# Kernel optimization log

Hardware: AMD Instinct MI355X
Metric: run time of the kernel (lower is better)

The kernel has to match this reference:

```python
import jax, jax.numpy as jnp
import numpy as np

T, H, I, E, TOPK = 4096, 2880, 2880, 16, 4
EPS = 1e-5
ALPHA = 1.702


def setup_inputs() -> dict:
    key = jax.random.key(0)
    ks = jax.random.split(key, 8)
    s = 0.02
    return {
        "x": jax.random.normal(ks[0], (T, H), dtype=jnp.float32),
        "norm_w": jnp.ones((H,), dtype=jnp.float32),
        "gate_w": jax.random.normal(ks[1], (E, H), dtype=jnp.float32) * s,
        "gate_b": jax.random.normal(ks[2], (E,), dtype=jnp.float32) * s,
        "w1": jax.random.normal(ks[3], (E, 2 * I, H), dtype=jnp.float32) * s,  # fused gate_up
        "b1": jax.random.normal(ks[4], (E, 2 * I), dtype=jnp.float32) * s,
        "w2": jax.random.normal(ks[5], (E, H, I), dtype=jnp.float32) * s,      # down proj
        "b2": jax.random.normal(ks[6], (E, H), dtype=jnp.float32) * s,
    }


def _rmsnorm(x, w, eps=EPS):
    var = jnp.mean(x * x, axis=-1, keepdims=True)
    return x * jax.lax.rsqrt(var + eps) * w


def _swiglu(gu):
    glu, lin = jnp.split(gu, 2, axis=-1)
    return glu * jax.nn.sigmoid(ALPHA * glu) * (lin + 1.0)


def reference(x, norm_w, gate_w, gate_b, w1, b1, w2, b2):
    t = _rmsnorm(x, norm_w)                       # [T, H]
    logits = t @ gate_w.T + gate_b                # [T, E]
    # Renormalize routing: top-k of logits, softmax over the k selected logits
    vals, idx = jax.lax.top_k(logits, TOPK)       # [T, k]
    wts = jax.nn.softmax(vals, axis=-1)           # [T, k]
    combine = jnp.zeros((t.shape[0], E), dtype=t.dtype)
    combine = combine.at[jnp.arange(t.shape[0])[:, None], idx].set(wts)  # [T, E]
    out = jnp.zeros_like(x)
    for e in range(E):                            # small fixed expert loop
        gu = t @ w1[e].T + b1[e]                  # [T, 2I]
        y = _swiglu(gu) @ w2[e].T + b2[e]         # [T, H]
        out = out + combine[:, e:e + 1] * y
    return x + out
```

## Files before the change

kernel.cpp:

```cpp
#include <hip/hip_runtime.h>
#include <hip/hip_bf16.h>
#include <math.h>
#include <stdint.h>

#define T_TOK 4096
#define H_DIM 2880
#define E_NUM 16
#define ALPHA 1.702f
#define EPS_RMS 1e-5f

#define PADM 192
#define BK 32
#define NK (H_DIM / BK)
#define MAX_RT 104
#define MAX_ROWS (MAX_RT * PADM)
#define NCT1 30
#define NCT2 15
#define G1 (MAX_RT * NCT1)
#define G2 (MAX_RT * NCT2)

typedef __attribute__((ext_vector_type(8))) short short8;
typedef __attribute__((ext_vector_type(4))) float f32x4;

__device__ __forceinline__ unsigned short f2bf(float f) {
  unsigned u = __float_as_uint(f);
  return (unsigned short)((u + 0x7fffu + ((u >> 16) & 1u)) >> 16);
}
__device__ __forceinline__ unsigned pk2(float a, float b) {
  return (unsigned)f2bf(a) | ((unsigned)f2bf(b) << 16);
}
__device__ __forceinline__ void gl_lds16(const void* g, unsigned char* lds_dst) {
  __builtin_amdgcn_global_load_lds(
      (const __attribute__((address_space(1))) void*)g,
      (__attribute__((address_space(3))) void*)lds_dst, 16, 0, 0);
}

__global__ __launch_bounds__(256) void k_norm_gate(
    const float* __restrict__ x, const float* __restrict__ norm_w,
    const float* __restrict__ gate_w, const float* __restrict__ gate_b,
    float* __restrict__ out, unsigned short* __restrict__ t_out,
    int* __restrict__ topk_id, float* __restrict__ topk_w,
    int* __restrict__ counts)
{
  int t = blockIdx.x, tid = threadIdx.x;
  const float4* xr = (const float4*)(x + (size_t)t * H_DIM);
  float4* outr = (float4*)(out + (size_t)t * H_DIM);
  float4 xa[3];
  float ss = 0.f;
  int j = 0;
  for (int i = tid; i < 720; i += 256, j++) {
    float4 v = xr[i]; xa[j] = v; outr[i] = v;
    ss += v.x * v.x + v.y * v.y + v.z * v.z + v.w * v.w;
  }
#pragma unroll
  for (int o = 1; o < 64; o <<= 1) ss += __shfl_xor(ss, o, 64);
  __shared__ float red[4];
  if ((tid & 63) == 0) red[tid >> 6] = ss;
  __syncthreads();
  float rs = rsqrtf((red[0] + red[1] + red[2] + red[3]) * (1.f / H_DIM) + EPS_RMS);

  float part[16];
#pragma unroll
  for (int q = 0; q < 16; q++) part[q] = 0.f;
  j = 0;
  for (int i = tid; i < 720; i += 256, j++) {
    float4 v = xa[j];
    float4 w = ((const float4*)norm_w)[i];
    float t0 = v.x * rs * w.x, t1 = v.y * rs * w.y;
    float t2 = v.z * rs * w.z, t3 = v.w * rs * w.w;
    ushort4 b; b.x = f2bf(t0); b.y = f2bf(t1); b.z = f2bf(t2); b.w = f2bf(t3);
    ((ushort4*)(t_out + (size_t)t * H_DIM))[i] = b;
#pragma unroll
    for (int q = 0; q < 16; q++) {
      float4 g = ((const float4*)(gate_w + (size_t)q * H_DIM))[i];
      part[q] += t0 * g.x + t1 * g.y + t2 * g.z + t3 * g.w;
    }
  }
  __shared__ float lg[4][16];
#pragma unroll
  for (int q = 0; q < 16; q++) {
    float p = part[q];
#pragma unroll
    for (int o = 1; o < 64; o <<= 1) p += __shfl_xor(p, o, 64);
    if ((tid & 63) == 0) lg[tid >> 6][q] = p;
  }
  __syncthreads();
  if (tid == 0) {
    float logit[16];
    for (int q = 0; q < 16; q++)
      logit[q] = lg[0][q] + lg[1][q] + lg[2][q] + lg[3][q] + gate_b[q];
    unsigned used = 0; int idx[4]; float val[4];
    for (int k = 0; k < 4; k++) {
      float best = -3.4e38f; int bi = 0;
      for (int q = 0; q < 16; q++)
        if (!((used >> q) & 1u) && logit[q] > best) { best = logit[q]; bi = q; }
      used |= 1u << bi; idx[k] = bi; val[k] = best;
    }
    float s0 = 0.f, w4[4];
    for (int k = 0; k < 4; k++) { w4[k] = expf(val[k] - val[0]); s0 += w4[k]; }
    for (int k = 0; k < 4; k++) {
      topk_id[t * 4 + k] = idx[k];
      topk_w[t * 4 + k] = w4[k] / s0;
      atomicAdd(&counts[idx[k]], 1);
    }
  }
}

__global__ void k_offsets(const int* __restrict__ counts, int* __restrict__ d_off) {
  if (threadIdx.x == 0) {
    int acc = 0;
    for (int q = 0; q < 16; q++) {
      d_off[q] = acc;
      acc += ((counts[q] + PADM - 1) / PADM) * PADM;
    }
    d_off[16] = acc;
  }
}

__global__ __launch_bounds__(256) void k_fill(
    const int* __restrict__ topk_id, const float* __restrict__ topk_w,
    const int* __restrict__ counts, const int* __restrict__ d_off,
    int* __restrict__ perm_tok, float* __restrict__ perm_w)
{
  int e = blockIdx.x;
  int base = d_off[e], pe = d_off[e + 1] - base, cnt = counts[e];
  int tid = threadIdx.x, lane = tid & 63, wv = tid >> 6;
  __shared__ int wsum[4];
  int pos = 0;
  for (int c0 = 0; c0 < T_TOK; c0 += 256) {
    int tok = c0 + tid;
    int4 ids = ((const int4*)topk_id)[tok];
    int flag = 0, slot = 0;
    if (ids.x == e) { flag = 1; slot = 0; }
    else if (ids.y == e) { flag = 1; slot = 1; }
    else if (ids.z == e) { flag = 1; slot = 2; }
    else if (ids.w == e) { flag = 1; slot = 3; }
    unsigned long long b = __ballot(flag);
    int wprefix = __popcll(b & ((1ULL << lane) - 1ULL));
    if (lane == 0) wsum[wv] = __popcll(b);
    __syncthreads();
    int woff = 0;
    for (int i = 0; i < wv; i++) woff += wsum[i];
    int tot = wsum[0] + wsum[1] + wsum[2] + wsum[3];
    if (flag) {
      int p = base + pos + woff + wprefix;
      perm_tok[p] = tok;
      perm_w[p] = topk_w[tok * 4 + slot];
    }
    pos += tot;
    __syncthreads();
  }
  for (int i = cnt + tid; i < pe; i += 256) {
    perm_tok[base + i] = 0;
    perm_w[base + i] = 0.f;
  }
}

__global__ __launch_bounds__(256, 2) void k_gemm1(
    const unsigned short* __restrict__ t_bf16,
    const float* __restrict__ w1, const float* __restrict__ b1,
    const int* __restrict__ perm_tok, const int* __restrict__ d_off,
    unsigned short* __restrict__ act)
{
  __shared__ __align__(16) unsigned char lds[49152];
  const int total = d_off[16];
  int bid = blockIdx.x;
  int wg = (bid & 7) * (G1 / 8) + (bid >> 3);
  int ct = wg / MAX_RT, rt = wg % MAX_RT;
  int rowbase = rt * PADM;
  if (rowbase >= total) return;
  int e = 0;
#pragma unroll
  for (int q = 0; q < E_NUM; q++) if (d_off[q + 1] <= rowbase) e = q + 1;

  int tid = threadIdx.x, lane = tid & 63, wv = tid >> 6;

  const unsigned short* asrc[3]; unsigned adst[3];
#pragma unroll
  for (int i = 0; i < 3; i++) {
    int cl = tid + 256 * i;
    int r = cl >> 2, c = cl & 3;
    int cs = c ^ ((r >> 1) & 3);
    int tok = perm_tok[rowbase + r];
    asrc[i] = t_bf16 + (size_t)tok * H_DIM + cs * 8;
    adst[i] = (unsigned)cl * 16;
  }
  const float4* bsrc[3]; unsigned bdst[3];
#pragma unroll
  for (int j = 0; j < 3; j++) {
    int idx = tid + 256 * j;
    int r = idx >> 2, c = idx & 3;
    size_t grow = (size_t)e * (2 * H_DIM) +
                  (r < 96 ? (size_t)(ct * 96 + r) : (size_t)(H_DIM + ct * 96 + (r - 96)));
    bsrc[j] = (const float4*)(w1 + grow * H_DIM) + c * 2;
    bdst[j] = (unsigned)(24576 + r * 64 + ((c ^ ((r >> 1) & 3)) << 4));
  }

  int ch = lane >> 4;
  unsigned aoff[3], boff[12];
#pragma unroll
  for (int m = 0; m < 3; m++) {
    int r = wv * 48 + m * 16 + (lane & 15);
    aoff[m] = (unsigned)(r * 64 + ((ch ^ ((r >> 1) & 3)) << 4));
  }
#pragma unroll
  for (int n = 0; n < 12; n++) {
    int r = n * 16 + (lane & 15);
    boff[n] = (unsigned)(24576 + r * 64 + ((ch ^ ((r >> 1) & 3)) << 4));
  }

  f32x4 zero = {0.f, 0.f, 0.f, 0.f};
  f32x4 acc[3][12];
#pragma unroll
  for (int m = 0; m < 3; m++)
#pragma unroll
    for (int n = 0; n < 12; n++) acc[m][n] = zero;

  float4 bv[3][2];
#pragma unroll
  for (int i = 0; i < 3; i++) gl_lds16(asrc[i], lds + adst[i]);
#pragma unroll
  for (int j = 0; j < 3; j++) { bv[j][0] = bsrc[j][0]; bv[j][1] = bsrc[j][1]; }
#pragma unroll
  for (int j = 0; j < 3; j++) {
    uint4 p;
    p.x = pk2(bv[j][0].x, bv[j][0].y); p.y = pk2(bv[j][0].z, bv[j][0].w);
    p.z = pk2(bv[j][1].x, bv[j][1].y); p.w = pk2(bv[j][1].z, bv[j][1].w);
    *(uint4*)(lds + bdst[j]) = p;
  }
  __syncthreads();

  int cur = 0;
  for (int kk = 0; kk < NK; kk++) {
    int nxt = cur ^ 1;
    if (kk + 1 < NK) {
#pragma unroll
      for (int i = 0; i < 3; i++)
        gl_lds16(asrc[i] + (size_t)(kk + 1) * BK, lds + nxt * 12288 + adst[i]);
#pragma unroll
      for (int j = 0; j < 3; j++) {
        bv[j][0] = bsrc[j][(kk + 1) * 8];
        bv[j][1] = bsrc[j][(kk + 1) * 8 + 1];
      }
    }
    const unsigned char* Ab = lds + cur * 12288;
    short8 a[3];
#pragma unroll
    for (int m = 0; m < 3; m++) a[m] = *(const short8*)(Ab + aoff[m]);
    __builtin_amdgcn_s_setprio(1);
#pragma unroll
    for (int n = 0; n < 12; n++) {
      short8 b = *(const short8*)(lds + cur * 12288 + boff[n]);
#pragma unroll
      for (int m = 0; m < 3; m++)
        acc[m][n] = __builtin_amdgcn_mfma_f32_16x16x32_bf16(a[m], b, acc[m][n], 0, 0, 0);
    }
    __builtin_amdgcn_s_setprio(0);
    if (kk + 1 < NK) {
#pragma unroll
      for (int j = 0; j < 3; j++) {
        uint4 p;
        p.x = pk2(bv[j][0].x, bv[j][0].y); p.y = pk2(bv[j][0].z, bv[j][0].w);
        p.z = pk2(bv[j][1].x, bv[j][1].y); p.w = pk2(bv[j][1].z, bv[j][1].w);
        *(uint4*)(lds + nxt * 12288 + bdst[j]) = p;
      }
    }
    __syncthreads();
    cur = nxt;
  }

  int colL = lane & 15, rq = lane >> 4;
#pragma unroll
  for (int m = 0; m < 3; m++) {
    int row0 = rowbase + wv * 48 + m * 16 + rq * 4;
#pragma unroll
    for (int n = 0; n < 6; n++) {
      int col = ct * 96 + n * 16 + colL;
      float bg = b1[(size_t)e * (2 * H_DIM) + col];
      float bl = b1[(size_t)e * (2 * H_DIM) + H_DIM + col];
#pragma unroll
      for (int j = 0; j < 4; j++) {
        float g = acc[m][n][j] + bg;
        float l = acc[m][n + 6][j] + bl;
        float s = 1.f / (1.f + __expf(-ALPHA * g));
        act[(size_t)(row0 + j) * H_DIM + col] = f2bf(g * s * (l + 1.f));
      }
    }
  }
}

__global__ __launch_bounds__(256, 2) void k_gemm2(
    const unsigned short* __restrict__ act,
    const float* __restrict__ w2, const float* __restrict__ b2,
    const int* __restrict__ perm_tok, const float* __restrict__ perm_w,
    const int* __restrict__ d_off,
    float* __restrict__ out)
{
  __shared__ __align__(16) unsigned char lds[49152];
  __shared__ int stok[PADM]; __shared__ float swt[PADM];
  const int total = d_off[16];
  int bid = blockIdx.x;
  int wg = (bid & 7) * (G2 / 8) + (bid >> 3);
  int ct = wg / MAX_RT, rt = wg % MAX_RT;
  int rowbase = rt * PADM;
  if (rowbase >= total) return;
  int e = 0;
#pragma unroll
  for (int q = 0; q < E_NUM; q++) if (d_off[q + 1] <= rowbase) e = q + 1;

  int tid = threadIdx.x, lane = tid & 63, wv = tid >> 6;
  if (tid < PADM) { stok[tid] = perm_tok[rowbase + tid]; swt[tid] = perm_w[rowbase + tid]; }

  const unsigned short* asrc[3]; unsigned adst[3];
#pragma unroll
  for (int i = 0; i < 3; i++) {
    int cl = tid + 256 * i;
    int r = cl >> 2, c = cl & 3;
    int cs = c ^ ((r >> 1) & 3);
    asrc[i] = act + (size_t)(rowbase + r) * H_DIM + cs * 8;
    adst[i] = (unsigned)cl * 16;
  }
  const float4* bsrc[3]; unsigned bdst[3];
#pragma unroll
  for (int j = 0; j < 3; j++) {
    int idx = tid + 256 * j;
    int r = idx >> 2, c = idx & 3;
    size_t grow = (size_t)e * H_DIM + (size_t)(ct * PADM + r);
    bsrc[j] = (const float4*)(w2 + grow * H_DIM) + c * 2;
    bdst[j] = (unsigned)(24576 + r * 64 + ((c ^ ((r >> 1) & 3)) << 4));
  }

  int ch = lane >> 4;
  unsigned aoff[3], boff[12];
#pragma unroll
  for (int m = 0; m < 3; m++) {
    int r = wv * 48 + m * 16 + (lane & 15);
    aoff[m] = (unsigned)(r * 64 + ((ch ^ ((r >> 1) & 3)) << 4));
  }
#pragma unroll
  for (int n = 0; n < 12; n++) {
    int r = n * 16 + (lane & 15);
    boff[n] = (unsigned)(24576 + r * 64 + ((ch ^ ((r >> 1) & 3)) << 4));
  }

  f32x4 zero = {0.f, 0.f, 0.f, 0.f};
  f32x4 acc[3][12];
#pragma unroll
  for (int m = 0; m < 3; m++)
#pragma unroll
    for (int n = 0; n < 12; n++) acc[m][n] = zero;

  float4 bv[3][2];
#pragma unroll
  for (int i = 0; i < 3; i++) gl_lds16(asrc[i], lds + adst[i]);
#pragma unroll
  for (int j = 0; j < 3; j++) { bv[j][0] = bsrc[j][0]; bv[j][1] = bsrc[j][1]; }
#pragma unroll
  for (int j = 0; j < 3; j++) {
    uint4 p;
    p.x = pk2(bv[j][0].x, bv[j][0].y); p.y = pk2(bv[j][0].z, bv[j][0].w);
    p.z = pk2(bv[j][1].x, bv[j][1].y); p.w = pk2(bv[j][1].z, bv[j][1].w);
    *(uint4*)(lds + bdst[j]) = p;
  }
  __syncthreads();

  int cur = 0;
  for (int kk = 0; kk < NK; kk++) {
    int nxt = cur ^ 1;
    if (kk + 1 < NK) {
#pragma unroll
      for (int i = 0; i < 3; i++)
        gl_lds16(asrc[i] + (size_t)(kk + 1) * BK, lds + nxt * 12288 + adst[i]);
#pragma unroll
      for (int j = 0; j < 3; j++) {
        bv[j][0] = bsrc[j][(kk + 1) * 8];
        bv[j][1] = bsrc[j][(kk + 1) * 8 + 1];
      }
    }
    const unsigned char* Ab = lds + cur * 12288;
    short8 a[3];
#pragma unroll
    for (int m = 0; m < 3; m++) a[m] = *(const short8*)(Ab + aoff[m]);
    __builtin_amdgcn_s_setprio(1);
#pragma unroll
    for (int n = 0; n < 12; n++) {
      short8 b = *(const short8*)(lds + cur * 12288 + boff[n]);
#pragma unroll
      for (int m = 0; m < 3; m++)
        acc[m][n] = __builtin_amdgcn_mfma_f32_16x16x32_bf16(a[m], b, acc[m][n], 0, 0, 0);
    }
    __builtin_amdgcn_s_setprio(0);
    if (kk + 1 < NK) {
#pragma unroll
      for (int j = 0; j < 3; j++) {
        uint4 p;
        p.x = pk2(bv[j][0].x, bv[j][0].y); p.y = pk2(bv[j][0].z, bv[j][0].w);
        p.z = pk2(bv[j][1].x, bv[j][1].y); p.w = pk2(bv[j][1].z, bv[j][1].w);
        *(uint4*)(lds + nxt * 12288 + bdst[j]) = p;
      }
    }
    __syncthreads();
    cur = nxt;
  }

  int colL = lane & 15, rq = lane >> 4;
#pragma unroll
  for (int m = 0; m < 3; m++) {
    int rl0 = wv * 48 + m * 16 + rq * 4;
#pragma unroll
    for (int n = 0; n < 12; n++) {
      int col = ct * PADM + n * 16 + colL;
      float bvv = b2[(size_t)e * H_DIM + col];
#pragma unroll
      for (int j = 0; j < 4; j++) {
        int rl = rl0 + j;
        float w = swt[rl];
        if (w != 0.f)
          atomicAdd(out + (size_t)stok[rl] * H_DIM + col, (acc[m][n][j] + bvv) * w);
      }
    }
  }
}

extern "C" void kernel_launch(void* const* d_in, const int* in_sizes, int n_in,
                              void* d_out, int out_size, void* d_ws, size_t ws_size,
                              hipStream_t stream)
{
  const float* x      = (const float*)d_in[0];
  const float* norm_w = (const float*)d_in[1];
  const float* gate_w = (const float*)d_in[2];
  const float* gate_b = (const float*)d_in[3];
  const float* w1     = (const float*)d_in[4];
  const float* b1     = (const float*)d_in[5];
  const float* w2     = (const float*)d_in[6];
  const float* b2     = (const float*)d_in[7];
  float* out = (float*)d_out;
  char* ws = (char*)d_ws;

  unsigned short* t_bf16  = (unsigned short*)(ws);
  unsigned short* act     = (unsigned short*)(ws + 23592960);
  int*            topk_id = (int*)(ws + 138608640);
  float*          topk_w  = (float*)(ws + 138674176);
  int*            perm_tk = (int*)(ws + 138739712);
  float*          perm_w  = (float*)(ws + 138819584);
  int*            counts  = (int*)(ws + 138899456);
  int*            d_off   = (int*)(ws + 138899520);

  hipMemsetAsync(counts, 0, 64, stream);
  hipLaunchKernelGGL(k_norm_gate, dim3(T_TOK), dim3(256), 0, stream,
                     x, norm_w, gate_w, gate_b, out, t_bf16, topk_id, topk_w, counts);
  hipLaunchKernelGGL(k_offsets, dim3(1), dim3(64), 0, stream, counts, d_off);
  hipLaunchKernelGGL(k_fill, dim3(16), dim3(256), 0, stream,
                     topk_id, topk_w, counts, d_off, perm_tk, perm_w);
  hipLaunchKernelGGL(k_gemm1, dim3(G1), dim3(256), 0, stream,
                     t_bf16, w1, b1, perm_tk, d_off, act);
  hipLaunchKernelGGL(k_gemm2, dim3(G2), dim3(256), 0, stream,
                     act, w2, b2, perm_tk, perm_w, d_off, out);
}
```

Baseline: 1.762 ms.

## Retile MoE GEMMs to 256-row, 512-thread blocks with BK=64 phased pipeline

```diff
diff --git a/kernel.cpp b/kernel.cpp
--- a/kernel.cpp
+++ b/kernel.cpp
@@ -9,15 +9,16 @@
 #define ALPHA 1.702f
 #define EPS_RMS 1e-5f
 
-#define PADM 192
-#define BK 32
-#define NK (H_DIM / BK)
-#define MAX_RT 104
+#define PADM 256
+#define BK 64
+#define NKT (H_DIM / BK)
+#define MAX_RT 80
 #define MAX_ROWS (MAX_RT * PADM)
 #define NCT1 30
 #define NCT2 15
 #define G1 (MAX_RT * NCT1)
 #define G2 (MAX_RT * NCT2)
+#define LBUF 57344
 
 typedef __attribute__((ext_vector_type(8))) short short8;
 typedef __attribute__((ext_vector_type(4))) float f32x4;
@@ -34,6 +35,8 @@
       (const __attribute__((address_space(1))) void*)g,
       (__attribute__((address_space(3))) void*)lds_dst, 16, 0, 0);
 }
+#define BARS() do { __builtin_amdgcn_s_barrier(); __builtin_amdgcn_sched_barrier(0); } while (0)
+#define DRAIN() asm volatile("s_waitcnt vmcnt(0) lgkmcnt(0)" ::: "memory")
 
 __global__ __launch_bounds__(256) void k_norm_gate(
     const float* __restrict__ x, const float* __restrict__ norm_w,
@@ -156,13 +159,65 @@
   }
 }
 
-__global__ __launch_bounds__(256, 2) void k_gemm1(
+#define PH_G1(H, MH, STAGE, POST)                                                   \
+  {                                                                                 \
+    const unsigned char* Ab = lds + cur * LBUF;                                     \
+    int r0 = wm * 64 + (MH) * 32 + lr;                                              \
+    unsigned ko = (unsigned)((((H) * 4 + lh) ^ S) << 4);                            \
+    short8 a0 = *(const short8*)(Ab + r0 * 128 + ko);                               \
+    short8 a1 = *(const short8*)(Ab + (r0 + 16) * 128 + ko);                        \
+    if ((MH) == 0) {                                                                \
+      _Pragma("unroll")                                                             \
+      for (int nf = 0; nf < 3; nf++) {                                              \
+        unsigned bo = (unsigned)((wn * 48 + nf * 16 + lr) * 128) + ko;              \
+        bgf[nf] = *(const short8*)(Ab + 32768 + bo);                                \
+        blf[nf] = *(const short8*)(Ab + 45056 + bo);                                \
+      }                                                                             \
+    }                                                                               \
+    STAGE;                                                                          \
+    BARS();                                                                         \
+    __builtin_amdgcn_s_setprio(1);                                                  \
+    _Pragma("unroll")                                                               \
+    for (int nf = 0; nf < 3; nf++) {                                                \
+      acc[0][(MH)*2][nf]   = __builtin_amdgcn_mfma_f32_16x16x32_bf16(a0, bgf[nf], acc[0][(MH)*2][nf], 0, 0, 0);   \
+      acc[0][(MH)*2+1][nf] = __builtin_amdgcn_mfma_f32_16x16x32_bf16(a1, bgf[nf], acc[0][(MH)*2+1][nf], 0, 0, 0); \
+      acc[1][(MH)*2][nf]   = __builtin_amdgcn_mfma_f32_16x16x32_bf16(a0, blf[nf], acc[1][(MH)*2][nf], 0, 0, 0);   \
+      acc[1][(MH)*2+1][nf] = __builtin_amdgcn_mfma_f32_16x16x32_bf16(a1, blf[nf], acc[1][(MH)*2+1][nf], 0, 0, 0); \
+    }                                                                               \
+    __builtin_amdgcn_s_setprio(0);                                                  \
+    POST;                                                                           \
+    BARS();                                                                         \
+  }
+
+#define G1_ST_BLOAD do { if (st) {                                                  \
+  _Pragma("unroll")                                                                 \
+  for (int j = 0; j < 3; j++) {                                                     \
+    bv[j][0] = bptr[j][(kt + 1) * 16];                                              \
+    bv[j][1] = bptr[j][(kt + 1) * 16 + 1];                                          \
+  } } } while (0)
+
+#define G1_ST_AGLD do { if (st) {                                                   \
+  _Pragma("unroll")                                                                 \
+  for (int i = 0; i < 4; i++)                                                       \
+    gl_lds16(aptr[i] + (size_t)(kt + 1) * BK, lds + nxt * LBUF + adst[i]);          \
+  } } while (0)
+
+#define G1_ST_BPACK do { if (st) {                                                  \
+  _Pragma("unroll")                                                                 \
+  for (int j = 0; j < 3; j++) {                                                     \
+    uint4 p;                                                                        \
+    p.x = pk2(bv[j][0].x, bv[j][0].y); p.y = pk2(bv[j][0].z, bv[j][0].w);           \
+    p.z = pk2(bv[j][1].x, bv[j][1].y); p.w = pk2(bv[j][1].z, bv[j][1].w);           \
+    *(uint4*)(lds + nxt * LBUF + bdst[j]) = p;                                      \
+  } } } while (0)
+
+__global__ __launch_bounds__(512, 2) void k_gemm1(
     const unsigned short* __restrict__ t_bf16,
     const float* __restrict__ w1, const float* __restrict__ b1,
     const int* __restrict__ perm_tok, const int* __restrict__ d_off,
     unsigned short* __restrict__ act)
 {
-  __shared__ __align__(16) unsigned char lds[49152];
+  __shared__ __align__(16) unsigned char lds[2 * LBUF];
   const int total = d_off[16];
   int bid = blockIdx.x;
   int wg = (bid & 7) * (G1 / 8) + (bid >> 3);
@@ -173,54 +228,46 @@
 #pragma unroll
   for (int q = 0; q < E_NUM; q++) if (d_off[q + 1] <= rowbase) e = q + 1;
 
-  int tid = threadIdx.x, lane = tid & 63, wv = tid >> 6;
-
-  const unsigned short* asrc[3]; unsigned adst[3];
-#pragma unroll
-  for (int i = 0; i < 3; i++) {
-    int cl = tid + 256 * i;
-    int r = cl >> 2, c = cl & 3;
-    int cs = c ^ ((r >> 1) & 3);
+  int tid = threadIdx.x, lane = tid & 63;
+  int wv = tid >> 6, wm = wv & 3, wn = wv >> 2;
+  int lr = lane & 15, lh = lane >> 4, S = lane & 7;
+
+  const unsigned short* aptr[4]; unsigned adst[4];
+#pragma unroll
+  for (int i = 0; i < 4; i++) {
+    int ch = tid + 512 * i;
+    int r = ch >> 3, c = ch & 7;
     int tok = perm_tok[rowbase + r];
-    asrc[i] = t_bf16 + (size_t)tok * H_DIM + cs * 8;
-    adst[i] = (unsigned)cl * 16;
-  }
-  const float4* bsrc[3]; unsigned bdst[3];
+    aptr[i] = t_bf16 + (size_t)tok * H_DIM + ((c ^ (r & 7)) * 8);
+    adst[i] = (unsigned)ch * 16;
+  }
+  const float4* bptr[3]; unsigned bdst[3];
 #pragma unroll
   for (int j = 0; j < 3; j++) {
-    int idx = tid + 256 * j;
-    int r = idx >> 2, c = idx & 3;
-    size_t grow = (size_t)e * (2 * H_DIM) +
-                  (r < 96 ? (size_t)(ct * 96 + r) : (size_t)(H_DIM + ct * 96 + (r - 96)));
-    bsrc[j] = (const float4*)(w1 + grow * H_DIM) + c * 2;
-    bdst[j] = (unsigned)(24576 + r * 64 + ((c ^ ((r >> 1) & 3)) << 4));
-  }
-
-  int ch = lane >> 4;
-  unsigned aoff[3], boff[12];
-#pragma unroll
-  for (int m = 0; m < 3; m++) {
-    int r = wv * 48 + m * 16 + (lane & 15);
-    aoff[m] = (unsigned)(r * 64 + ((ch ^ ((r >> 1) & 3)) << 4));
-  }
-#pragma unroll
-  for (int n = 0; n < 12; n++) {
-    int r = n * 16 + (lane & 15);
-    boff[n] = (unsigned)(24576 + r * 64 + ((ch ^ ((r >> 1) & 3)) << 4));
+    int ch = tid + 512 * j;
+    int half = ch >= 768;
+    int rr = (ch - half * 768) >> 3, c = ch & 7;
+    size_t grow = (size_t)e * (2 * H_DIM) + (size_t)(ct * 96 + rr) + (size_t)half * H_DIM;
+    bptr[j] = (const float4*)(w1 + grow * H_DIM) + c * 2;
+    bdst[j] = (unsigned)(32768 + half * 12288 + rr * 128 + ((c ^ (rr & 7)) << 4));
   }
 
   f32x4 zero = {0.f, 0.f, 0.f, 0.f};
-  f32x4 acc[3][12];
-#pragma unroll
-  for (int m = 0; m < 3; m++)
-#pragma unroll
-    for (int n = 0; n < 12; n++) acc[m][n] = zero;
-
+  f32x4 acc[2][4][3];
+#pragma unroll
+  for (int p = 0; p < 2; p++)
+#pragma unroll
+    for (int m = 0; m < 4; m++)
+#pragma unroll
+      for (int n = 0; n < 3; n++) acc[p][m][n] = zero;
+
+  short8 bgf[3], blf[3];
   float4 bv[3][2];
-#pragma unroll
-  for (int i = 0; i < 3; i++) gl_lds16(asrc[i], lds + adst[i]);
-#pragma unroll
-  for (int j = 0; j < 3; j++) { bv[j][0] = bsrc[j][0]; bv[j][1] = bsrc[j][1]; }
+
+#pragma unroll
+  for (int j = 0; j < 3; j++) { bv[j][0] = bptr[j][0]; bv[j][1] = bptr[j][1]; }
+#pragma unroll
+  for (int i = 0; i < 4; i++) gl_lds16(aptr[i], lds + adst[i]);
 #pragma unroll
   for (int j = 0; j < 3; j++) {
     uint4 p;
@@ -228,60 +275,31 @@
     p.z = pk2(bv[j][1].x, bv[j][1].y); p.w = pk2(bv[j][1].z, bv[j][1].w);
     *(uint4*)(lds + bdst[j]) = p;
   }
-  __syncthreads();
-
-  int cur = 0;
-  for (int kk = 0; kk < NK; kk++) {
-    int nxt = cur ^ 1;
-    if (kk + 1 < NK) {
-#pragma unroll
-      for (int i = 0; i < 3; i++)
-        gl_lds16(asrc[i] + (size_t)(kk + 1) * BK, lds + nxt * 12288 + adst[i]);
-#pragma unroll
-      for (int j = 0; j < 3; j++) {
-        bv[j][0] = bsrc[j][(kk + 1) * 8];
-        bv[j][1] = bsrc[j][(kk + 1) * 8 + 1];
-      }
-    }
-    const unsigned char* Ab = lds + cur * 12288;
-    short8 a[3];
-#pragma unroll
-    for (int m = 0; m < 3; m++) a[m] = *(const short8*)(Ab + aoff[m]);
-    __builtin_amdgcn_s_setprio(1);
-#pragma unroll
-    for (int n = 0; n < 12; n++) {
-      short8 b = *(const short8*)(lds + cur * 12288 + boff[n]);
-#pragma unroll
-      for (int m = 0; m < 3; m++)
-        acc[m][n] = __builtin_amdgcn_mfma_f32_16x16x32_bf16(a[m], b, acc[m][n], 0, 0, 0);
-    }
-    __builtin_amdgcn_s_setprio(0);
-    if (kk + 1 < NK) {
-#pragma unroll
-      for (int j = 0; j < 3; j++) {
-        uint4 p;
-        p.x = pk2(bv[j][0].x, bv[j][0].y); p.y = pk2(bv[j][0].z, bv[j][0].w);
-        p.z = pk2(bv[j][1].x, bv[j][1].y); p.w = pk2(bv[j][1].z, bv[j][1].w);
-        *(uint4*)(lds + nxt * 12288 + bdst[j]) = p;
-      }
-    }
-    __syncthreads();
-    cur = nxt;
-  }
-
-  int colL = lane & 15, rq = lane >> 4;
-#pragma unroll
-  for (int m = 0; m < 3; m++) {
-    int row0 = rowbase + wv * 48 + m * 16 + rq * 4;
-#pragma unroll
-    for (int n = 0; n < 6; n++) {
-      int col = ct * 96 + n * 16 + colL;
+  DRAIN();
+  BARS();
+
+#pragma unroll 1
+  for (int kt = 0; kt < NKT; kt++) {
+    int cur = kt & 1, nxt = cur ^ 1;
+    bool st = (kt + 1 < NKT);
+    PH_G1(0, 0, G1_ST_BLOAD, );
+    PH_G1(0, 1, G1_ST_AGLD, );
+    PH_G1(1, 0, G1_ST_BPACK, );
+    PH_G1(1, 1, , DRAIN());
+  }
+
+#pragma unroll
+  for (int mf = 0; mf < 4; mf++) {
+    int row0 = rowbase + wm * 64 + mf * 16 + lh * 4;
+#pragma unroll
+    for (int nf = 0; nf < 3; nf++) {
+      int col = ct * 96 + wn * 48 + nf * 16 + lr;
       float bg = b1[(size_t)e * (2 * H_DIM) + col];
       float bl = b1[(size_t)e * (2 * H_DIM) + H_DIM + col];
 #pragma unroll
       for (int j = 0; j < 4; j++) {
-        float g = acc[m][n][j] + bg;
-        float l = acc[m][n + 6][j] + bl;
+        float g = acc[0][mf][nf][j] + bg;
+        float l = acc[1][mf][nf][j] + bl;
         float s = 1.f / (1.f + __expf(-ALPHA * g));
         act[(size_t)(row0 + j) * H_DIM + col] = f2bf(g * s * (l + 1.f));
       }
@@ -289,14 +307,41 @@
   }
 }
 
-__global__ __launch_bounds__(256, 2) void k_gemm2(
+#define PH_G2(H, MH, STAGE, POST)                                                   \
+  {                                                                                 \
+    const unsigned char* Ab = lds + cur * LBUF;                                     \
+    int r0 = wm * 64 + (MH) * 32 + lr;                                              \
+    unsigned ko = (unsigned)((((H) * 4 + lh) ^ S) << 4);                            \
+    short8 a0 = *(const short8*)(Ab + r0 * 128 + ko);                               \
+    short8 a1 = *(const short8*)(Ab + (r0 + 16) * 128 + ko);                        \
+    if ((MH) == 0) {                                                                \
+      _Pragma("unroll")                                                             \
+      for (int nf = 0; nf < 6; nf++) {                                              \
+        unsigned bo = (unsigned)((wn * 96 + nf * 16 + lr) * 128) + ko;              \
+        bf[nf] = *(const short8*)(Ab + 32768 + bo);                                 \
+      }                                                                             \
+    }                                                                               \
+    STAGE;                                                                          \
+    BARS();                                                                         \
+    __builtin_amdgcn_s_setprio(1);                                                  \
+    _Pragma("unroll")                                                               \
+    for (int nf = 0; nf < 6; nf++) {                                                \
+      acc[(MH)*2][nf]   = __builtin_amdgcn_mfma_f32_16x16x32_bf16(a0, bf[nf], acc[(MH)*2][nf], 0, 0, 0);   \
+      acc[(MH)*2+1][nf] = __builtin_amdgcn_mfma_f32_16x16x32_bf16(a1, bf[nf], acc[(MH)*2+1][nf], 0, 0, 0); \
+    }                                                                               \
+    __builtin_amdgcn_s_setprio(0);                                                  \
+    POST;                                                                           \
+    BARS();                                                                         \
+  }
+
+__global__ __launch_bounds__(512, 2) void k_gemm2(
     const unsigned short* __restrict__ act,
     const float* __restrict__ w2, const float* __restrict__ b2,
     const int* __restrict__ perm_tok, const float* __restrict__ perm_w,
     const int* __restrict__ d_off,
     float* __restrict__ out)
 {
-  __shared__ __align__(16) unsigned char lds[49152];
+  __shared__ __align__(16) unsigned char lds[2 * LBUF];
   __shared__ int stok[PADM]; __shared__ float swt[PADM];
   const int total = d_off[16];
   int bid = blockIdx.x;
@@ -308,53 +353,44 @@
 #pragma unroll
   for (int q = 0; q < E_NUM; q++) if (d_off[q + 1] <= rowbase) e = q + 1;
 
-  int tid = threadIdx.x, lane = tid & 63, wv = tid >> 6;
+  int tid = threadIdx.x, lane = tid & 63;
+  int wv = tid >> 6, wm = wv & 3, wn = wv >> 2;
+  int lr = lane & 15, lh = lane >> 4, S = lane & 7;
+
   if (tid < PADM) { stok[tid] = perm_tok[rowbase + tid]; swt[tid] = perm_w[rowbase + tid]; }
 
-  const unsigned short* asrc[3]; unsigned adst[3];
-#pragma unroll
-  for (int i = 0; i < 3; i++) {
-    int cl = tid + 256 * i;
-    int r = cl >> 2, c = cl & 3;
-    int cs = c ^ ((r >> 1) & 3);
-    asrc[i] = act + (size_t)(rowbase + r) * H_DIM + cs * 8;
-    adst[i] = (unsigned)cl * 16;
-  }
-  const float4* bsrc[3]; unsigned bdst[3];
+  const unsigned short* aptr[4]; unsigned adst[4];
+#pragma unroll
+  for (int i = 0; i < 4; i++) {
+    int ch = tid + 512 * i;
+    int r = ch >> 3, c = ch & 7;
+    aptr[i] = act + (size_t)(rowbase + r) * H_DIM + ((c ^ (r & 7)) * 8);
+    adst[i] = (unsigned)ch * 16;
+  }
+  const float4* bptr[3]; unsigned bdst[3];
 #pragma unroll
   for (int j = 0; j < 3; j++) {
-    int idx = tid + 256 * j;
-    int r = idx >> 2, c = idx & 3;
-    size_t grow = (size_t)e * H_DIM + (size_t)(ct * PADM + r);
-    bsrc[j] = (const float4*)(w2 + grow * H_DIM) + c * 2;
-    bdst[j] = (unsigned)(24576 + r * 64 + ((c ^ ((r >> 1) & 3)) << 4));
-  }
-
-  int ch = lane >> 4;
-  unsigned aoff[3], boff[12];
-#pragma unroll
-  for (int m = 0; m < 3; m++) {
-    int r = wv * 48 + m * 16 + (lane & 15);
-    aoff[m] = (unsigned)(r * 64 + ((ch ^ ((r >> 1) & 3)) << 4));
-  }
-#pragma unroll
-  for (int n = 0; n < 12; n++) {
-    int r = n * 16 + (lane & 15);
-    boff[n] = (unsigned)(24576 + r * 64 + ((ch ^ ((r >> 1) & 3)) << 4));
+    int ch = tid + 512 * j;
+    int rr = ch >> 3, c = ch & 7;
+    size_t grow = (size_t)e * H_DIM + (size_t)(ct * 192 + rr);
+    bptr[j] = (const float4*)(w2 + grow * H_DIM) + c * 2;
+    bdst[j] = (unsigned)(32768 + rr * 128 + ((c ^ (rr & 7)) << 4));
   }
 
   f32x4 zero = {0.f, 0.f, 0.f, 0.f};
-  f32x4 acc[3][12];
-#pragma unroll
-  for (int m = 0; m < 3; m++)
-#pragma unroll
-    for (int n = 0; n < 12; n++) acc[m][n] = zero;
-
+  f32x4 acc[4][6];
+#pragma unroll
+  for (int m = 0; m < 4; m++)
+#pragma unroll
+    for (int n = 0; n < 6; n++) acc[m][n] = zero;
+
+  short8 bf[6];
   float4 bv[3][2];
-#pragma unroll
-  for (int i = 0; i < 3; i++) gl_lds16(asrc[i], lds + adst[i]);
-#pragma unroll
-  for (int j = 0; j < 3; j++) { bv[j][0] = bsrc[j][0]; bv[j][1] = bsrc[j][1]; }
+
+#pragma unroll
+  for (int j = 0; j < 3; j++) { bv[j][0] = bptr[j][0]; bv[j][1] = bptr[j][1]; }
+#pragma unroll
+  for (int i = 0; i < 4; i++) gl_lds16(aptr[i], lds + adst[i]);
 #pragma unroll
   for (int j = 0; j < 3; j++) {
     uint4 p;
@@ -362,61 +398,32 @@
     p.z = pk2(bv[j][1].x, bv[j][1].y); p.w = pk2(bv[j][1].z, bv[j][1].w);
     *(uint4*)(lds + bdst[j]) = p;
   }
-  __syncthreads();
-
-  int cur = 0;
-  for (int kk = 0; kk < NK; kk++) {
-    int nxt = cur ^ 1;
-    if (kk + 1 < NK) {
-#pragma unroll
-      for (int i = 0; i < 3; i++)
-        gl_lds16(asrc[i] + (size_t)(kk + 1) * BK, lds + nxt * 12288 + adst[i]);
-#pragma unroll
-      for (int j = 0; j < 3; j++) {
-        bv[j][0] = bsrc[j][(kk + 1) * 8];
-        bv[j][1] = bsrc[j][(kk + 1) * 8 + 1];
-      }
-    }
-    const unsigned char* Ab = lds + cur * 12288;
-    short8 a[3];
-#pragma unroll
-    for (int m = 0; m < 3; m++) a[m] = *(const short8*)(Ab + aoff[m]);
-    __builtin_amdgcn_s_setprio(1);
-#pragma unroll
-    for (int n = 0; n < 12; n++) {
-      short8 b = *(const short8*)(lds + cur * 12288 + boff[n]);
-#pragma unroll
-      for (int m = 0; m < 3; m++)
-        acc[m][n] = __builtin_amdgcn_mfma_f32_16x16x32_bf16(a[m], b, acc[m][n], 0, 0, 0);
-    }
-    __builtin_amdgcn_s_setprio(0);
-    if (kk + 1 < NK) {
-#pragma unroll
-      for (int j = 0; j < 3; j++) {
-        uint4 p;
-        p.x = pk2(bv[j][0].x, bv[j][0].y); p.y = pk2(bv[j][0].z, bv[j][0].w);
-        p.z = pk2(bv[j][1].x, bv[j][1].y); p.w = pk2(bv[j][1].z, bv[j][1].w);
-        *(uint4*)(lds + nxt * 12288 + bdst[j]) = p;
-      }
-    }
-    __syncthreads();
-    cur = nxt;
-  }
-
-  int colL = lane & 15, rq = lane >> 4;
-#pragma unroll
-  for (int m = 0; m < 3; m++) {
-    int rl0 = wv * 48 + m * 16 + rq * 4;
-#pragma unroll
-    for (int n = 0; n < 12; n++) {
-      int col = ct * PADM + n * 16 + colL;
-      float bvv = b2[(size_t)e * H_DIM + col];
+  DRAIN();
+  BARS();
+
+#pragma unroll 1
+  for (int kt = 0; kt < NKT; kt++) {
+    int cur = kt & 1, nxt = cur ^ 1;
+    bool st = (kt + 1 < NKT);
+    PH_G2(0, 0, G1_ST_BLOAD, );
+    PH_G2(0, 1, G1_ST_AGLD, );
+    PH_G2(1, 0, G1_ST_BPACK, );
+    PH_G2(1, 1, , DRAIN());
+  }
+
+#pragma unroll
+  for (int mf = 0; mf < 4; mf++) {
+    int rl0 = wm * 64 + mf * 16 + lh * 4;
+#pragma unroll
+    for (int nf = 0; nf < 6; nf++) {
+      int col = ct * 192 + wn * 96 + nf * 16 + lr;
+      float b2v = b2[(size_t)e * H_DIM + col];
 #pragma unroll
       for (int j = 0; j < 4; j++) {
         int rl = rl0 + j;
         float w = swt[rl];
         if (w != 0.f)
-          atomicAdd(out + (size_t)stok[rl] * H_DIM + col, (acc[m][n][j] + bvv) * w);
+          atomicAdd(out + (size_t)stok[rl] * H_DIM + col, (acc[mf][nf][j] + b2v) * w);
       }
     }
   }
@@ -439,12 +446,12 @@
 
   unsigned short* t_bf16  = (unsigned short*)(ws);
   unsigned short* act     = (unsigned short*)(ws + 23592960);
-  int*            topk_id = (int*)(ws + 138608640);
-  float*          topk_w  = (float*)(ws + 138674176);
-  int*            perm_tk = (int*)(ws + 138739712);
-  float*          perm_w  = (float*)(ws + 138819584);
-  int*            counts  = (int*)(ws + 138899456);
-  int*            d_off   = (int*)(ws + 138899520);
+  int*            topk_id = (int*)(ws + 141557760);
+  float*          topk_w  = (float*)(ws + 141623296);
+  int*            perm_tk = (int*)(ws + 141688832);
+  float*          perm_w  = (float*)(ws + 141770752);
+  int*            counts  = (int*)(ws + 141852672);
+  int*            d_off   = (int*)(ws + 141852736);
 
   hipMemsetAsync(counts, 0, 64, stream);
   hipLaunchKernelGGL(k_norm_gate, dim3(T_TOK), dim3(256), 0, stream,
@@ -452,8 +459,8 @@
   hipLaunchKernelGGL(k_offsets, dim3(1), dim3(64), 0, stream, counts, d_off);
   hipLaunchKernelGGL(k_fill, dim3(16), dim3(256), 0, stream,
                      topk_id, topk_w, counts, d_off, perm_tk, perm_w);
-  hipLaunchKernelGGL(k_gemm1, dim3(G1), dim3(256), 0, stream,
+  hipLaunchKernelGGL(k_gemm1, dim3(G1), dim3(512), 0, stream,
                      t_bf16, w1, b1, perm_tk, d_off, act);
-  hipLaunchKernelGGL(k_gemm2, dim3(G2), dim3(256), 0, stream,
+  hipLaunchKernelGGL(k_gemm2, dim3(G2), dim3(512), 0, stream,
                      act, w2, b2, perm_tk, perm_w, d_off, out);
 }
```

After: 2.252 ms. 1.28x slower.

## Deepen the expert GEMM K-loop into a three-stage LDS pipeline

Applied to the files above, without the earlier changes.

```diff
diff --git a/kernel.cpp b/kernel.cpp
--- a/kernel.cpp
+++ b/kernel.cpp
@@ -13,11 +13,13 @@
 #define BK 32
 #define NK (H_DIM / BK)
 #define MAX_RT 104
-#define MAX_ROWS (MAX_RT * PADM)
 #define NCT1 30
 #define NCT2 15
 #define G1 (MAX_RT * NCT1)
 #define G2 (MAX_RT * NCT2)
+#define ABUF 12288
+#define BBUF 12288
+#define BOFF 36864
 
 typedef __attribute__((ext_vector_type(8))) short short8;
 typedef __attribute__((ext_vector_type(4))) float f32x4;
@@ -34,6 +36,11 @@
       (const __attribute__((address_space(1))) void*)g,
       (__attribute__((address_space(3))) void*)lds_dst, 16, 0, 0);
 }
+#define ENDSTEP() do {                                           \
+    asm volatile("s_waitcnt lgkmcnt(0)" ::: "memory");           \
+    __builtin_amdgcn_s_barrier();                                \
+    __builtin_amdgcn_sched_barrier(0);                           \
+  } while (0)
 
 __global__ __launch_bounds__(256) void k_norm_gate(
     const float* __restrict__ x, const float* __restrict__ norm_w,
@@ -156,13 +163,78 @@
   }
 }
 
+#define STAGE_A(dstbuf, ktn) do {                                             \
+  _Pragma("unroll")                                                           \
+  for (int i = 0; i < 3; i++)                                                 \
+    gl_lds16(aptr[i] + (size_t)(ktn) * BK, lds + (dstbuf) * ABUF + adst[i]);  \
+} while (0)
+
+#define LOAD_B(set, ktn) do {                                                 \
+  _Pragma("unroll")                                                           \
+  for (int j = 0; j < 3; j++) {                                               \
+    set[j][0] = bptr[j][(ktn) * 8];                                           \
+    set[j][1] = bptr[j][(ktn) * 8 + 1];                                       \
+  }                                                                           \
+} while (0)
+
+#define PACK_B(set, dstbuf) do {                                              \
+  _Pragma("unroll")                                                           \
+  for (int j = 0; j < 3; j++) {                                               \
+    uint4 p;                                                                  \
+    p.x = pk2(set[j][0].x, set[j][0].y); p.y = pk2(set[j][0].z, set[j][0].w); \
+    p.z = pk2(set[j][1].x, set[j][1].y); p.w = pk2(set[j][1].z, set[j][1].w); \
+    *(uint4*)(lds + BOFF + (dstbuf) * BBUF + bdst[j]) = p;                    \
+  }                                                                           \
+} while (0)
+
+#define COMPUTE(cb) do {                                                      \
+  const unsigned char* Abase = lds + (cb) * ABUF + abase_off;                 \
+  const unsigned char* Bbase = lds + BOFF + (cb) * BBUF + bbase_off;          \
+  short8 a0 = *(const short8*)(Abase);                                        \
+  short8 a1 = *(const short8*)(Abase + 1024);                                 \
+  short8 a2 = *(const short8*)(Abase + 2048);                                 \
+  __builtin_amdgcn_s_setprio(1);                                              \
+  _Pragma("unroll")                                                           \
+  for (int n = 0; n < 12; n++) {                                              \
+    short8 b = *(const short8*)(Bbase + n * 1024);                            \
+    acc[0][n] = __builtin_amdgcn_mfma_f32_16x16x32_bf16(a0, b, acc[0][n], 0, 0, 0); \
+    acc[1][n] = __builtin_amdgcn_mfma_f32_16x16x32_bf16(a1, b, acc[1][n], 0, 0, 0); \
+    acc[2][n] = __builtin_amdgcn_mfma_f32_16x16x32_bf16(a2, b, acc[2][n], 0, 0, 0); \
+  }                                                                           \
+  __builtin_amdgcn_s_setprio(0);                                              \
+} while (0)
+
+#define GEMM_PIPE() do {                                                      \
+                                    \
+  STAGE_A(0, 0); LOAD_B(bv0, 0);                                              \
+  STAGE_A(1, 1); LOAD_B(bv1, 1);                                              \
+  PACK_B(bv0, 0);                                                             \
+  ENDSTEP();                                                                  \
+  int c0 = 0;                                                                 \
+  _Pragma("unroll 1")                                                         \
+  for (int u = 0; u < NK / 2; u++) {                                          \
+    int kt0 = 2 * u;                                                          \
+    int c1 = c0 + 1; if (c1 >= 3) c1 -= 3;                                    \
+    int c2 = c0 + 2; if (c2 >= 3) c2 -= 3;                                    \
+    if (kt0 + 2 < NK) { STAGE_A(c2, kt0 + 2); LOAD_B(bv0, kt0 + 2); }         \
+    COMPUTE(c0);                                                              \
+    PACK_B(bv1, c1);                                                          \
+    ENDSTEP();                                                                \
+    if (kt0 + 3 < NK) { STAGE_A(c0, kt0 + 3); LOAD_B(bv1, kt0 + 3); }         \
+    COMPUTE(c1);                                                              \
+    if (kt0 + 2 < NK) PACK_B(bv0, c2);                                        \
+    ENDSTEP();                                                                \
+    c0 = c2;                                                                  \
+  }                                                                           \
+} while (0)
+
 __global__ __launch_bounds__(256, 2) void k_gemm1(
     const unsigned short* __restrict__ t_bf16,
     const float* __restrict__ w1, const float* __restrict__ b1,
     const int* __restrict__ perm_tok, const int* __restrict__ d_off,
     unsigned short* __restrict__ act)
 {
-  __shared__ __align__(16) unsigned char lds[49152];
+  __shared__ __align__(16) unsigned char lds[3 * ABUF + 3 * BBUF];
   const int total = d_off[16];
   int bid = blockIdx.x;
   int wg = (bid & 7) * (G1 / 8) + (bid >> 3);
@@ -174,39 +246,29 @@
   for (int q = 0; q < E_NUM; q++) if (d_off[q + 1] <= rowbase) e = q + 1;
 
   int tid = threadIdx.x, lane = tid & 63, wv = tid >> 6;
-
-  const unsigned short* asrc[3]; unsigned adst[3];
+  int lr = lane & 15, ch = lane >> 4;
+  unsigned swz16 = (unsigned)((ch ^ ((lr >> 1) & 3)) << 4);
+  unsigned abase_off = (unsigned)(wv * 3072 + lr * 64) + swz16;
+  unsigned bbase_off = (unsigned)(lr * 64) + swz16;
+
+  const unsigned short* aptr[3]; unsigned adst[3];
 #pragma unroll
   for (int i = 0; i < 3; i++) {
     int cl = tid + 256 * i;
     int r = cl >> 2, c = cl & 3;
-    int cs = c ^ ((r >> 1) & 3);
     int tok = perm_tok[rowbase + r];
-    asrc[i] = t_bf16 + (size_t)tok * H_DIM + cs * 8;
+    aptr[i] = t_bf16 + (size_t)tok * H_DIM + ((c ^ ((r >> 1) & 3)) * 8);
     adst[i] = (unsigned)cl * 16;
   }
-  const float4* bsrc[3]; unsigned bdst[3];
+  const float4* bptr[3]; unsigned bdst[3];
 #pragma unroll
   for (int j = 0; j < 3; j++) {
     int idx = tid + 256 * j;
-    int r = idx >> 2, c = idx & 3;
+    int rr = idx >> 2, c = idx & 3;
     size_t grow = (size_t)e * (2 * H_DIM) +
-                  (r < 96 ? (size_t)(ct * 96 + r) : (size_t)(H_DIM + ct * 96 + (r - 96)));
-    bsrc[j] = (const float4*)(w1 + grow * H_DIM) + c * 2;
-    bdst[j] = (unsigned)(24576 + r * 64 + ((c ^ ((r >> 1) & 3)) << 4));
-  }
-
-  int ch = lane >> 4;
-  unsigned aoff[3], boff[12];
-#pragma unroll
-  for (int m = 0; m < 3; m++) {
-    int r = wv * 48 + m * 16 + (lane & 15);
-    aoff[m] = (unsigned)(r * 64 + ((ch ^ ((r >> 1) & 3)) << 4));
-  }
-#pragma unroll
-  for (int n = 0; n < 12; n++) {
-    int r = n * 16 + (lane & 15);
-    boff[n] = (unsigned)(24576 + r * 64 + ((ch ^ ((r >> 1) & 3)) << 4));
+                  (rr < 96 ? (size_t)(ct * 96 + rr) : (size_t)(H_DIM + ct * 96 + (rr - 96)));
+    bptr[j] = (const float4*)(w1 + grow * H_DIM) + c * 2;
+    bdst[j] = (unsigned)(rr * 64 + ((c ^ ((rr >> 1) & 3)) << 4));
   }
 
   f32x4 zero = {0.f, 0.f, 0.f, 0.f};
@@ -215,67 +277,17 @@
   for (int m = 0; m < 3; m++)
 #pragma unroll
     for (int n = 0; n < 12; n++) acc[m][n] = zero;
-
-  float4 bv[3][2];
-#pragma unroll
-  for (int i = 0; i < 3; i++) gl_lds16(asrc[i], lds + adst[i]);
-#pragma unroll
-  for (int j = 0; j < 3; j++) { bv[j][0] = bsrc[j][0]; bv[j][1] = bsrc[j][1]; }
-#pragma unroll
-  for (int j = 0; j < 3; j++) {
-    uint4 p;
-    p.x = pk2(bv[j][0].x, bv[j][0].y); p.y = pk2(bv[j][0].z, bv[j][0].w);
-    p.z = pk2(bv[j][1].x, bv[j][1].y); p.w = pk2(bv[j][1].z, bv[j][1].w);
-    *(uint4*)(lds + bdst[j]) = p;
-  }
-  __syncthreads();
-
-  int cur = 0;
-  for (int kk = 0; kk < NK; kk++) {
-    int nxt = cur ^ 1;
-    if (kk + 1 < NK) {
-#pragma unroll
-      for (int i = 0; i < 3; i++)
-        gl_lds16(asrc[i] + (size_t)(kk + 1) * BK, lds + nxt * 12288 + adst[i]);
-#pragma unroll
-      for (int j = 0; j < 3; j++) {
-        bv[j][0] = bsrc[j][(kk + 1) * 8];
-        bv[j][1] = bsrc[j][(kk + 1) * 8 + 1];
-      }
-    }
-    const unsigned char* Ab = lds + cur * 12288;
-    short8 a[3];
-#pragma unroll
-    for (int m = 0; m < 3; m++) a[m] = *(const short8*)(Ab + aoff[m]);
-    __builtin_amdgcn_s_setprio(1);
-#pragma unroll
-    for (int n = 0; n < 12; n++) {
-      short8 b = *(const short8*)(lds + cur * 12288 + boff[n]);
-#pragma unroll
-      for (int m = 0; m < 3; m++)
-        acc[m][n] = __builtin_amdgcn_mfma_f32_16x16x32_bf16(a[m], b, acc[m][n], 0, 0, 0);
-    }
-    __builtin_amdgcn_s_setprio(0);
-    if (kk + 1 < NK) {
-#pragma unroll
-      for (int j = 0; j < 3; j++) {
-        uint4 p;
-        p.x = pk2(bv[j][0].x, bv[j][0].y); p.y = pk2(bv[j][0].z, bv[j][0].w);
-        p.z = pk2(bv[j][1].x, bv[j][1].y); p.w = pk2(bv[j][1].z, bv[j][1].w);
-        *(uint4*)(lds + nxt * 12288 + bdst[j]) = p;
-      }
-    }
-    __syncthreads();
-    cur = nxt;
-  }
-
-  int colL = lane & 15, rq = lane >> 4;
+  float4 bv0[3][2], bv1[3][2];
+
+  GEMM_PIPE();
+
+  int rq = lane >> 4;
 #pragma unroll
   for (int m = 0; m < 3; m++) {
     int row0 = rowbase + wv * 48 + m * 16 + rq * 4;
 #pragma unroll
     for (int n = 0; n < 6; n++) {
-      int col = ct * 96 + n * 16 + colL;
+      int col = ct * 96 + n * 16 + lr;
       float bg = b1[(size_t)e * (2 * H_DIM) + col];
       float bl = b1[(size_t)e * (2 * H_DIM) + H_DIM + col];
 #pragma unroll
@@ -296,7 +308,7 @@
     const int* __restrict__ d_off,
     float* __restrict__ out)
 {
-  __shared__ __align__(16) unsigned char lds[49152];
+  __shared__ __align__(16) unsigned char lds[3 * ABUF + 3 * BBUF];
   __shared__ int stok[PADM]; __shared__ float swt[PADM];
   const int total = d_off[16];
   int bid = blockIdx.x;
@@ -309,38 +321,29 @@
   for (int q = 0; q < E_NUM; q++) if (d_off[q + 1] <= rowbase) e = q + 1;
 
   int tid = threadIdx.x, lane = tid & 63, wv = tid >> 6;
+  int lr = lane & 15, ch = lane >> 4;
+  unsigned swz16 = (unsigned)((ch ^ ((lr >> 1) & 3)) << 4);
+  unsigned abase_off = (unsigned)(wv * 3072 + lr * 64) + swz16;
+  unsigned bbase_off = (unsigned)(lr * 64) + swz16;
+
   if (tid < PADM) { stok[tid] = perm_tok[rowbase + tid]; swt[tid] = perm_w[rowbase + tid]; }
 
-  const unsigned short* asrc[3]; unsigned adst[3];
+  const unsigned short* aptr[3]; unsigned adst[3];
 #pragma unroll
   for (int i = 0; i < 3; i++) {
     int cl = tid + 256 * i;
     int r = cl >> 2, c = cl & 3;
-    int cs = c ^ ((r >> 1) & 3);
-    asrc[i] = act + (size_t)(rowbase + r) * H_DIM + cs * 8;
+    aptr[i] = act + (size_t)(rowbase + r) * H_DIM + ((c ^ ((r >> 1) & 3)) * 8);
     adst[i] = (unsigned)cl * 16;
   }
-  const float4* bsrc[3]; unsigned bdst[3];
+  const float4* bptr[3]; unsigned bdst[3];
 #pragma unroll
   for (int j = 0; j < 3; j++) {
     int idx = tid + 256 * j;
-    int r = idx >> 2, c = idx & 3;
-    size_t grow = (size_t)e * H_DIM + (size_t)(ct * PADM + r);
-    bsrc[j] = (const float4*)(w2 + grow * H_DIM) + c * 2;
-    bdst[j] = (unsigned)(24576 + r * 64 + ((c ^ ((r >> 1) & 3)) << 4));
-  }
-
-  int ch = lane >> 4;
-  unsigned aoff[3], boff[12];
-#pragma unroll
-  for (int m = 0; m < 3; m++) {
-    int r = wv * 48 + m * 16 + (lane & 15);
-    aoff[m] = (unsigned)(r * 64 + ((ch ^ ((r >> 1) & 3)) << 4));
-  }
-#pragma unroll
-  for (int n = 0; n < 12; n++) {
-    int r = n * 16 + (lane & 15);
-    boff[n] = (unsigned)(24576 + r * 64 + ((ch ^ ((r >> 1) & 3)) << 4));
+    int rr = idx >> 2, c = idx & 3;
+    size_t grow = (size_t)e * H_DIM + (size_t)(ct * 192 + rr);
+    bptr[j] = (const float4*)(w2 + grow * H_DIM) + c * 2;
+    bdst[j] = (unsigned)(rr * 64 + ((c ^ ((rr >> 1) & 3)) << 4));
   }
 
   f32x4 zero = {0.f, 0.f, 0.f, 0.f};
@@ -349,74 +352,24 @@
   for (int m = 0; m < 3; m++)
 #pragma unroll
     for (int n = 0; n < 12; n++) acc[m][n] = zero;
-
-  float4 bv[3][2];
-#pragma unroll
-  for (int i = 0; i < 3; i++) gl_lds16(asrc[i], lds + adst[i]);
-#pragma unroll
-  for (int j = 0; j < 3; j++) { bv[j][0] = bsrc[j][0]; bv[j][1] = bsrc[j][1]; }
-#pragma unroll
-  for (int j = 0; j < 3; j++) {
-    uint4 p;
-    p.x = pk2(bv[j][0].x, bv[j][0].y); p.y = pk2(bv[j][0].z, bv[j][0].w);
-    p.z = pk2(bv[j][1].x, bv[j][1].y); p.w = pk2(bv[j][1].z, bv[j][1].w);
-    *(uint4*)(lds + bdst[j]) = p;
-  }
-  __syncthreads();
-
-  int cur = 0;
-  for (int kk = 0; kk < NK; kk++) {
-    int nxt = cur ^ 1;
-    if (kk + 1 < NK) {
-#pragma unroll
-      for (int i = 0; i < 3; i++)
-        gl_lds16(asrc[i] + (size_t)(kk + 1) * BK, lds + nxt * 12288 + adst[i]);
-#pragma unroll
-      for (int j = 0; j < 3; j++) {
-        bv[j][0] = bsrc[j][(kk + 1) * 8];
-        bv[j][1] = bsrc[j][(kk + 1) * 8 + 1];
-      }
-    }
-    const unsigned char* Ab = lds + cur * 12288;
-    short8 a[3];
-#pragma unroll
-    for (int m = 0; m < 3; m++) a[m] = *(const short8*)(Ab + aoff[m]);
-    __builtin_amdgcn_s_setprio(1);
-#pragma unroll
-    for (int n = 0; n < 12; n++) {
-      short8 b = *(const short8*)(lds + cur * 12288 + boff[n]);
-#pragma unroll
-      for (int m = 0; m < 3; m++)
-        acc[m][n] = __builtin_amdgcn_mfma_f32_16x16x32_bf16(a[m], b, acc[m][n], 0, 0, 0);
-    }
-    __builtin_amdgcn_s_setprio(0);
-    if (kk + 1 < NK) {
-#pragma unroll
-      for (int j = 0; j < 3; j++) {
-        uint4 p;
-        p.x = pk2(bv[j][0].x, bv[j][0].y); p.y = pk2(bv[j][0].z, bv[j][0].w);
-        p.z = pk2(bv[j][1].x, bv[j][1].y); p.w = pk2(bv[j][1].z, bv[j][1].w);
-        *(uint4*)(lds + nxt * 12288 + bdst[j]) = p;
-      }
-    }
-    __syncthreads();
-    cur = nxt;
-  }
-
-  int colL = lane & 15, rq = lane >> 4;
+  float4 bv0[3][2], bv1[3][2];
+
+  GEMM_PIPE();
+
+  int rq = lane >> 4;
 #pragma unroll
   for (int m = 0; m < 3; m++) {
     int rl0 = wv * 48 + m * 16 + rq * 4;
 #pragma unroll
     for (int n = 0; n < 12; n++) {
-      int col = ct * PADM + n * 16 + colL;
-      float bvv = b2[(size_t)e * H_DIM + col];
+      int col = ct * 192 + n * 16 + lr;
+      float b2v = b2[(size_t)e * H_DIM + col];
 #pragma unroll
       for (int j = 0; j < 4; j++) {
         int rl = rl0 + j;
         float w = swt[rl];
         if (w != 0.f)
-          atomicAdd(out + (size_t)stok[rl] * H_DIM + col, (acc[m][n][j] + bvv) * w);
+          atomicAdd(out + (size_t)stok[rl] * H_DIM + col, (acc[m][n][j] + b2v) * w);
       }
     }
   }
```

New measurement: 2.874 ms. +63.1%, slower.
